# Kernel optimization log

Hardware: AMD Instinct MI355X
Metric: run time of the kernel (lower is better)

Reference implementation:

```python
import jax, jax.numpy as jnp
import numpy as np


def setup_inputs() -> dict:
    key = jax.random.key(0)
    ks = jax.random.split(key, 8)
    B, Cin, Cattr, Cout, H, W = 8, 256, 256, 256, 64, 64
    x = jax.random.normal(ks[0], (B, Cin, H, W), dtype=jnp.float32)
    attr = jax.random.normal(ks[1], (B, Cattr, H, W), dtype=jnp.float32)
    # 1x1 conv weights stored as [out, in] (kernel_size=1 squeezed)
    sq = 1.0 / np.sqrt(Cin)
    sa = 1.0 / np.sqrt(Cattr)
    Wq = jax.random.uniform(ks[2], (Cout, Cin), jnp.float32, -sq, sq)
    bq = jax.random.uniform(ks[3], (Cout,), jnp.float32, -sq, sq)
    Wk = jax.random.uniform(ks[4], (Cout, Cattr), jnp.float32, -sa, sa)
    bk = jax.random.uniform(ks[5], (Cout,), jnp.float32, -sa, sa)
    Wv = jax.random.uniform(ks[6], (Cout, Cattr), jnp.float32, -sa, sa)
    bv = jax.random.uniform(ks[7], (Cout,), jnp.float32, -sa, sa)
    return {"x": x, "attr": attr, "Wq": Wq, "bq": bq, "Wk": Wk, "bk": bk, "Wv": Wv, "bv": bv}


def reference(x, attr, Wq, bq, Wk, bk, Wv, bv):
    B, Cin, H, W = x.shape
    # 1x1 convs == per-pixel linear projections
    q = jnp.einsum('bchw,oc->bohw', x, Wq) + bq[None, :, None, None]      # [B,C,H,W]
    k = jnp.einsum('bchw,oc->bohw', attr, Wk) + bk[None, :, None, None]
    v = jnp.einsum('bchw,oc->bohw', attr, Wv) + bv[None, :, None, None]
    C = q.shape[1]
    qf = q.reshape(B, C, H * W)   # [B,C,N]
    kf = k.reshape(B, C, H * W)
    vf = v.reshape(B, C, H * W)
    # attn[b,i,j] = sum_c q[b,c,i] * k[b,c,j]  -> softmax over j
    attn = jax.nn.softmax(jnp.einsum('bci,bcj->bij', qf, kf), axis=-1)    # [B,N,N]
    out = jnp.einsum('bcj,bij->bci', vf, attn)                            # [B,C,N]
    return out.reshape(B, C, H, W) + x
```

## Files before the change

kernel.cpp:

```cpp
#include <hip/hip_runtime.h>

typedef _Float16 f16;
typedef _Float16 f16x8 __attribute__((ext_vector_type(8)));
typedef _Float16 f16x4 __attribute__((ext_vector_type(4)));
typedef float f32x4 __attribute__((ext_vector_type(4)));
typedef float f32x16 __attribute__((ext_vector_type(16)));

#define LOG2E 1.44269504088896340736f
#define SOFF  36.0f
#define CDIM 256
#define NPIX 4096

__device__ __forceinline__ void gl2lds16(const f16* g, const f16* l) {
    __builtin_amdgcn_global_load_lds((const __attribute__((address_space(1))) unsigned int*)g,
                                     (__attribute__((address_space(3))) unsigned int*)l, 16, 0, 0);
}

__global__ void convert_w_kernel(const float* __restrict__ Wq, const float* __restrict__ Wk,
                                 const float* __restrict__ Wv,
                                 f16* __restrict__ WqF, f16* __restrict__ WkF,
                                 f16* __restrict__ WvF) {
    int t = blockIdx.x * 256 + threadIdx.x;
    int m = t >> 13;
    int g = t & 8191;
    int lane = g & 63;
    int ksct = g >> 6;
    int ks = ksct & 15, ct = ksct >> 4;
    int o = ct * 32 + (lane & 31);
    int cin0 = ks * 16 + (lane >> 5) * 8;
    const float* W = (m == 0) ? Wq : ((m == 1) ? Wk : Wv);
    f16* WF = (m == 0) ? WqF : ((m == 1) ? WkF : WvF);
    const float scale = (m == 0) ? LOG2E : 1.0f;
    const float* src = W + (size_t)o * CDIM + cin0;
    f16x8 v;
#pragma unroll
    for (int e = 0; e < 8; ++e) v[e] = (f16)(src[e] * scale);
    *(f16x8*)(WF + (size_t)g * 8) = v;
}

__global__ __launch_bounds__(256, 2)
void proj_kernel(const float* __restrict__ x, const float* __restrict__ attr,
                 const f16* __restrict__ WqF, const float* __restrict__ bq,
                 const f16* __restrict__ WkF, const float* __restrict__ bk,
                 const f16* __restrict__ WvF, const float* __restrict__ bv,
                 f16* __restrict__ qT, f16* __restrict__ kT, f16* __restrict__ vF) {
    __shared__ __align__(16) f16 Xs[64 * 256];
    __shared__ __align__(16) f16 As[64 * 256];

    const int b  = blockIdx.x & 7;
    const int i0 = (blockIdx.x >> 3) * 64;
    const int t  = threadIdx.x;
    const int w = t >> 6, lane = t & 63, l31 = lane & 31, hi = lane >> 5;
    const int xorv = l31 & 7;

    {
        const int i  = t & 63;
        const int cb = t >> 6;
        const float* xb = x    + (size_t)b * CDIM * NPIX + i0 + i;
        const float* ab = attr + (size_t)b * CDIM * NPIX + i0 + i;
#pragma unroll 2
        for (int rep = 0; rep < 8; ++rep) {
            int chunk = cb * 8 + rep;
            const float* xs = xb + (size_t)(chunk * 8) * NPIX;
            const float* as_ = ab + (size_t)(chunk * 8) * NPIX;
            f16x8 xv, av;
#pragma unroll
            for (int e = 0; e < 8; ++e) {
                xv[e] = (f16)xs[(size_t)e * NPIX];
                av[e] = (f16)as_[(size_t)e * NPIX];
            }
            int phys = chunk ^ (i & 7);
            *(f16x8*)(Xs + i * 256 + phys * 8) = xv;
            *(f16x8*)(As + i * 256 + phys * 8) = av;
        }
    }
    __syncthreads();

#pragma unroll 1
    for (int k = 0; k < 12; ++k) {
        const int tt = w + 4 * k;
        const int kind = tt >> 4;
        const int rr = tt & 15;
        const int ct = rr >> 1;
        const int half = rr & 1;

        const f16* WF = (kind == 0) ? WqF : ((kind == 1) ? WkF : WvF);
        const f16* Bs = (kind == 0) ? Xs : As;
        const float* bias = (kind == 0) ? bq : ((kind == 1) ? bk : bv);
        const float bscale = (kind == 0) ? LOG2E : 1.0f;

        const f16* ap = WF + (size_t)(ct * 16) * 512 + (size_t)lane * 8;
        const f16* bp = Bs + (half * 32 + l31) * 256;

        f32x16 acc;
#pragma unroll
        for (int r = 0; r < 16; ++r) acc[r] = 0.0f;
#pragma unroll
        for (int ks = 0; ks < 16; ++ks) {
            f16x8 afr = *(const f16x8*)(ap + ks * 512);
            f16x8 bfr = *(const f16x8*)(bp + (((2 * ks + hi) ^ xorv)) * 8);
            acc = __builtin_amdgcn_mfma_f32_32x32x16_f16(afr, bfr, acc, 0, 0, 0);
        }

        const int nidx = i0 + half * 32 + l31;
        if (kind < 2) {
            f16* dst = ((kind == 0) ? qT : kT)
                       + ((size_t)b * NPIX + nidx) * CDIM + ct * 32 + 4 * hi;
#pragma unroll
            for (int g = 0; g < 4; ++g) {
                f32x4 bb = *(const f32x4*)(bias + ct * 32 + 4 * hi + 8 * g);
                f16x4 pk;
#pragma unroll
                for (int e = 0; e < 4; ++e) pk[e] = (f16)(acc[4 * g + e] + bb[e] * bscale);
                *(f16x4*)(dst + 8 * g) = pk;
            }
        } else {
            const int jpart = ((nidx >> 4) << 9) + (((nidx >> 3) & 1) << 8) + (nidx & 7);
            f16* vb2 = vF + (size_t)b * CDIM * NPIX + (size_t)ct * 131072 + jpart;
#pragma unroll
            for (int g = 0; g < 4; ++g) {
                f32x4 bb = *(const f32x4*)(bias + ct * 32 + 4 * hi + 8 * g);
#pragma unroll
                for (int e = 0; e < 4; ++e) {
                    int c31 = 4 * hi + 8 * g + e;
                    vb2[c31 * 8] = (f16)(acc[4 * g + e] + bb[e]);
                }
            }
        }
    }
}

__global__ __launch_bounds__(512, 2)
void attn_kernel(const f16* __restrict__ qT, const f16* __restrict__ kT,
                 const f16* __restrict__ vF, const float* __restrict__ x,
                 float* __restrict__ out) {
    extern __shared__ unsigned char smem[];

    const int b    = blockIdx.x & 7;
    const int i0   = (blockIdx.x >> 3) * 128;
    const int t    = threadIdx.x;
    const int w    = t >> 6;
    const int lane = t & 63;
    const int l31  = lane & 31;
    const int hi   = lane >> 5;
    const int iw   = (w & 3) * 32;
    const int jh   = (w >> 2) * 32;
    const int jh16 = (w >> 2) * 2;
    const int ig   = i0 + iw + l31;
    const int xorv = l31 & 7;

    f16x8 qf[16];
    {
        const f16* qp = qT + ((size_t)b * NPIX + ig) * CDIM + hi * 8;
#pragma unroll
        for (int ks = 0; ks < 16; ++ks) qf[ks] = *(const f16x8*)(qp + ks * 16);
    }

    int kp4o[4];
    {
        int kboff = (jh + l31) * 256 + (hi ^ (xorv & 1)) * 8;
        const int xv2 = xorv >> 1;
#pragma unroll
        for (int r = 0; r < 4; ++r) kp4o[r] = kboff + (r ^ xv2) * 16;
    }

    f32x16 acc[8];
#pragma unroll
    for (int ct = 0; ct < 8; ++ct)
#pragma unroll
        for (int r = 0; r < 16; ++r) acc[ct][r] = 0.0f;
    float lrun = 0.0f;

    const f16* kb  = kT + (size_t)b * NPIX * CDIM;
    const f16* vbJ = vF + (size_t)b * CDIM * NPIX;
    f16* lds0 = (f16*)smem;
    const int wub = (t & ~63) * 8;

    {
#pragma unroll
        for (int rep = 0; rep < 4; ++rep) {
            int slot = t + rep * 512;
            int krow = slot >> 5, kpc = slot & 31;
            gl2lds16(kb + (size_t)krow * CDIM + ((kpc ^ (krow & 7)) * 8),
                     lds0 + wub + rep * 4096);
        }
    }

    union Q4 { f16x4 h; unsigned int u[2]; };
    union B8 { f16x8 h; unsigned int u[4]; };

#pragma unroll 1
    for (int jt = 0; jt < 64; ++jt) {
        const int p = jt & 1;
        __syncthreads();

        const f16* vjt = vbJ + (size_t)jt * 2048 + (lane << 3) + (jh16 << 9);
        f16x8 vx0 = *(const f16x8*)(vjt);
        f16x8 vx1 = *(const f16x8*)(vjt + 512);
        f16x8 vy0 = *(const f16x8*)(vjt + 131072);
        f16x8 vy1 = *(const f16x8*)(vjt + 131072 + 512);

        if (jt < 63) {
            const int j0n = (jt + 1) * 64;
            f16* dstb = lds0 + (p ^ 1) * 16384;
#pragma unroll
            for (int rep = 0; rep < 4; ++rep) {
                int slot = t + rep * 512;
                int krow = slot >> 5, kpc = slot & 31;
                gl2lds16(kb + (size_t)(j0n + krow) * CDIM + ((kpc ^ (krow & 7)) * 8),
                         dstb + wub + rep * 4096);
            }
        }

        const f16* L = lds0 + p * 16384;

        f32x16 s;
#pragma unroll
        for (int r = 0; r < 16; ++r) s[r] = -SOFF;
#pragma unroll
        for (int ks = 0; ks < 16; ++ks)
            s = __builtin_amdgcn_mfma_f32_32x32x16_f16(
                *(const f16x8*)(L + kp4o[ks & 3] + (ks >> 2) * 64), qf[ks], s, 0, 0, 0);

        Q4 ownq[4];
        float rtot = 0.0f;
#pragma unroll
        for (int g = 0; g < 4; ++g) {
            float p0 = __builtin_amdgcn_exp2f(s[4 * g + 0]);
            float p1 = __builtin_amdgcn_exp2f(s[4 * g + 1]);
            float p2 = __builtin_amdgcn_exp2f(s[4 * g + 2]);
            float p3 = __builtin_amdgcn_exp2f(s[4 * g + 3]);
            rtot += (p0 + p1) + (p2 + p3);
            ownq[g].h[0] = (f16)p0; ownq[g].h[1] = (f16)p1;
            ownq[g].h[2] = (f16)p2; ownq[g].h[3] = (f16)p3;
        }
        lrun += rtot;

        f16x8 pb[2];
#pragma unroll
        for (int kj = 0; kj < 2; ++kj) {
            int sidx = 2 * kj + 1 - hi;
            int oidx = 2 * kj + hi;
            unsigned int s0 = ownq[sidx].u[0], s1 = ownq[sidx].u[1];
            unsigned int r0 = (unsigned int)__shfl_xor((int)s0, 32);
            unsigned int r1 = (unsigned int)__shfl_xor((int)s1, 32);
            B8 bb;
            bb.u[0] = hi ? r0 : ownq[oidx].u[0];
            bb.u[1] = hi ? r1 : ownq[oidx].u[1];
            bb.u[2] = hi ? ownq[oidx].u[0] : r0;
            bb.u[3] = hi ? ownq[oidx].u[1] : r1;
            pb[kj] = bb.h;
        }

#pragma unroll
        for (int ct = 0; ct < 8; ++ct) {
            f16x8 c0 = (ct & 1) ? vy0 : vx0;
            f16x8 c1 = (ct & 1) ? vy1 : vx1;
            if (ct < 6) {
                const f16* np = vjt + (size_t)(ct + 2) * 131072;
                f16x8 n0 = *(const f16x8*)(np);
                f16x8 n1 = *(const f16x8*)(np + 512);
                if (ct & 1) { vy0 = n0; vy1 = n1; } else { vx0 = n0; vx1 = n1; }
            }
            acc[ct] = __builtin_amdgcn_mfma_f32_32x32x16_f16(c0, pb[0], acc[ct], 0, 0, 0);
            acc[ct] = __builtin_amdgcn_mfma_f32_32x32x16_f16(c1, pb[1], acc[ct], 0, 0, 0);
        }
    }

    float lsum = lrun + __shfl_xor(lrun, 32);
    __syncthreads();
    float* Obuf = (float*)smem;
    float* Ls   = (float*)(smem + 131072);
    if (w >= 4) {
        float* ob = Obuf + (w - 4) * 8192;
#pragma unroll
        for (int ct = 0; ct < 8; ++ct)
#pragma unroll
            for (int r = 0; r < 16; ++r) {
                int c = ct * 32 + (r & 3) + 8 * (r >> 2) + 4 * hi;
                ob[c * 32 + l31] = acc[ct][r];
            }
        if (hi == 0) Ls[(w - 4) * 32 + l31] = lsum;
    }
    __syncthreads();
    if (w < 4) {
        const float ltot = lsum + Ls[w * 32 + l31];
        const float invl = 1.0f / ltot;
        const float* po = Obuf + w * 8192;
        const float* xb = x + (size_t)b * CDIM * NPIX + i0 + iw;
        float* og = out + (size_t)b * CDIM * NPIX + i0 + iw;
#pragma unroll
        for (int ct = 0; ct < 8; ++ct)
#pragma unroll
            for (int r = 0; r < 16; ++r) {
                int c = ct * 32 + (r & 3) + 8 * (r >> 2) + 4 * hi;
                size_t off = (size_t)c * NPIX + l31;
                og[off] = (acc[ct][r] + po[c * 32 + l31]) * invl + xb[off];
            }
    }
}

extern "C" void kernel_launch(void* const* d_in, const int* in_sizes, int n_in,
                              void* d_out, int out_size, void* d_ws, size_t ws_size,
                              hipStream_t stream) {
    const float* x    = (const float*)d_in[0];
    const float* attr = (const float*)d_in[1];
    const float* Wq   = (const float*)d_in[2];
    const float* bq   = (const float*)d_in[3];
    const float* Wk   = (const float*)d_in[4];
    const float* bk   = (const float*)d_in[5];
    const float* Wv   = (const float*)d_in[6];
    const float* bv   = (const float*)d_in[7];
    float* out = (float*)d_out;

    char* ws = (char*)d_ws;
    const size_t qkv_bytes = (size_t)8 * NPIX * CDIM * sizeof(f16);
    f16* qT   = (f16*)ws;
    f16* kT   = (f16*)(ws + qkv_bytes);
    f16* vF   = (f16*)(ws + 2 * qkv_bytes);
    f16* WqF  = (f16*)(ws + 3 * qkv_bytes);
    f16* WkF  = WqF + 65536;
    f16* WvF  = WkF + 65536;

    (void)hipFuncSetAttribute((const void*)attn_kernel,
                              hipFuncAttributeMaxDynamicSharedMemorySize, 131584);

    convert_w_kernel<<<96, 256, 0, stream>>>(Wq, Wk, Wv, WqF, WkF, WvF);
    proj_kernel<<<512, 256, 0, stream>>>(x, attr, WqF, bq, WkF, bk, WvF, bv, qT, kT, vF);
    attn_kernel<<<256, 512, 131584, stream>>>(qT, kT, vF, x, out);
}
```

Measured before the change: 326.8 us.

## Stage V tiles through LDS double buffer and widen swizzles

V is now stored row-major [C,N] and loaded into LDS with async global-to-LDS copies alongside K, double-buffered per tile, instead of each wave reading pre-fragmented V directly from global memory. The XOR swizzle widens to 32 columns for K and the projection operands to reduce LDS bank conflicts, and the projection epilogue stages results in LDS so global writes are coalesced 16-byte stores. s_setprio brackets the MFMA loops. This doubles the LDS footprint per stage (within the existing 131584-byte allocation) and adds LDS read traffic for V.

```diff
diff --git a/kernel.cpp b/kernel.cpp
--- a/kernel.cpp
+++ b/kernel.cpp
@@ -43,15 +43,17 @@
                  const f16* __restrict__ WqF, const float* __restrict__ bq,
                  const f16* __restrict__ WkF, const float* __restrict__ bk,
                  const f16* __restrict__ WvF, const float* __restrict__ bv,
-                 f16* __restrict__ qT, f16* __restrict__ kT, f16* __restrict__ vF) {
+                 f16* __restrict__ qT, f16* __restrict__ kT, f16* __restrict__ vW) {
     __shared__ __align__(16) f16 Xs[64 * 256];
     __shared__ __align__(16) f16 As[64 * 256];
+    __shared__ __align__(16) f16 Ostage[4][1024];
 
     const int b  = blockIdx.x & 7;
     const int i0 = (blockIdx.x >> 3) * 64;
     const int t  = threadIdx.x;
     const int w = t >> 6, lane = t & 63, l31 = lane & 31, hi = lane >> 5;
-    const int xorv = l31 & 7;
+    const int xu  = (l31 >> 1) & 15;
+    const int hib = (hi ^ (l31 & 1)) * 8;
 
     {
         const int i  = t & 63;
@@ -69,7 +71,7 @@
                 xv[e] = (f16)xs[(size_t)e * NPIX];
                 av[e] = (f16)as_[(size_t)e * NPIX];
             }
-            int phys = chunk ^ (i & 7);
+            int phys = chunk ^ (i & 31);
             *(f16x8*)(Xs + i * 256 + phys * 8) = xv;
             *(f16x8*)(As + i * 256 + phys * 8) = av;
         }
@@ -90,7 +92,7 @@
         const float bscale = (kind == 0) ? LOG2E : 1.0f;
 
         const f16* ap = WF + (size_t)(ct * 16) * 512 + (size_t)lane * 8;
-        const f16* bp = Bs + (half * 32 + l31) * 256;
+        const f16* bp = Bs + (half * 32 + l31) * 256 + hib;
 
         f32x16 acc;
 #pragma unroll
@@ -98,33 +100,47 @@
 #pragma unroll
         for (int ks = 0; ks < 16; ++ks) {
             f16x8 afr = *(const f16x8*)(ap + ks * 512);
-            f16x8 bfr = *(const f16x8*)(bp + (((2 * ks + hi) ^ xorv)) * 8);
+            f16x8 bfr = *(const f16x8*)(bp + ((ks ^ xu) << 4));
             acc = __builtin_amdgcn_mfma_f32_32x32x16_f16(afr, bfr, acc, 0, 0, 0);
         }
 
-        const int nidx = i0 + half * 32 + l31;
+        f16* st = Ostage[w];
         if (kind < 2) {
-            f16* dst = ((kind == 0) ? qT : kT)
-                       + ((size_t)b * NPIX + nidx) * CDIM + ct * 32 + 4 * hi;
 #pragma unroll
             for (int g = 0; g < 4; ++g) {
                 f32x4 bb = *(const f32x4*)(bias + ct * 32 + 4 * hi + 8 * g);
                 f16x4 pk;
 #pragma unroll
                 for (int e = 0; e < 4; ++e) pk[e] = (f16)(acc[4 * g + e] + bb[e] * bscale);
-                *(f16x4*)(dst + 8 * g) = pk;
+                *(f16x4*)(st + l31 * 32 + 4 * hi + 8 * g) = pk;
+            }
+            f16* dst = ((kind == 0) ? qT : kT)
+                       + ((size_t)b * NPIX + i0 + half * 32) * CDIM + ct * 32;
+#pragma unroll
+            for (int d = 0; d < 2; ++d) {
+                int row = d * 16 + (lane >> 2);
+                int c8  = (lane & 3) * 8;
+                f16x8 v = *(const f16x8*)(st + row * 32 + c8);
+                *(f16x8*)(dst + (size_t)row * CDIM + c8) = v;
             }
         } else {
-            const int jpart = ((nidx >> 4) << 9) + (((nidx >> 3) & 1) << 8) + (nidx & 7);
-            f16* vb2 = vF + (size_t)b * CDIM * NPIX + (size_t)ct * 131072 + jpart;
 #pragma unroll
             for (int g = 0; g < 4; ++g) {
                 f32x4 bb = *(const f32x4*)(bias + ct * 32 + 4 * hi + 8 * g);
 #pragma unroll
                 for (int e = 0; e < 4; ++e) {
                     int c31 = 4 * hi + 8 * g + e;
-                    vb2[c31 * 8] = (f16)(acc[4 * g + e] + bb[e]);
+                    st[c31 * 32 + l31] = (f16)(acc[4 * g + e] + bb[e]);
                 }
+            }
+            const int j0 = i0 + half * 32;
+            f16* dstb = vW + (size_t)b * CDIM * NPIX + (size_t)(ct * 32) * NPIX + j0;
+#pragma unroll
+            for (int d = 0; d < 2; ++d) {
+                int chunk = d * 64 + lane;
+                int c31 = chunk >> 2, jch = chunk & 3;
+                *(f16x8*)(dstb + (size_t)c31 * NPIX + jch * 8) =
+                    *(const f16x8*)(st + chunk * 8);
             }
         }
     }
@@ -132,7 +148,7 @@
 
 __global__ __launch_bounds__(512, 2)
 void attn_kernel(const f16* __restrict__ qT, const f16* __restrict__ kT,
-                 const f16* __restrict__ vF, const float* __restrict__ x,
+                 const f16* __restrict__ vW, const float* __restrict__ x,
                  float* __restrict__ out) {
     extern __shared__ unsigned char smem[];
 
@@ -145,9 +161,8 @@
     const int hi   = lane >> 5;
     const int iw   = (w & 3) * 32;
     const int jh   = (w >> 2) * 32;
-    const int jh16 = (w >> 2) * 2;
+    const int jh8  = (w >> 2) * 4;
     const int ig   = i0 + iw + l31;
-    const int xorv = l31 & 7;
 
     f16x8 qf[16];
     {
@@ -156,12 +171,14 @@
         for (int ks = 0; ks < 16; ++ks) qf[ks] = *(const f16x8*)(qp + ks * 16);
     }
 
-    int kp4o[4];
+    const int xu  = (l31 >> 1) & 15;
+    const int kbase = (jh + l31) * 256 + (hi ^ (l31 & 1)) * 8;
+    int vp2o[2];
     {
-        int kboff = (jh + l31) * 256 + (hi ^ (xorv & 1)) * 8;
-        const int xv2 = xorv >> 1;
-#pragma unroll
-        for (int r = 0; r < 4; ++r) kp4o[r] = kboff + (r ^ xv2) * 16;
+        int vbase = 16384 + (l31 >> 2) * 256 + (l31 & 3) * 64;
+#pragma unroll
+        for (int kj = 0; kj < 2; ++kj)
+            vp2o[kj] = vbase + (((jh8 + 2 * kj + hi) ^ (l31 & 7))) * 8;
     }
 
     f32x16 acc[8];
@@ -171,8 +188,8 @@
         for (int r = 0; r < 16; ++r) acc[ct][r] = 0.0f;
     float lrun = 0.0f;
 
-    const f16* kb  = kT + (size_t)b * NPIX * CDIM;
-    const f16* vbJ = vF + (size_t)b * CDIM * NPIX;
+    const f16* kb = kT + (size_t)b * NPIX * CDIM;
+    const f16* vb = vW + (size_t)b * CDIM * NPIX;
     f16* lds0 = (f16*)smem;
     const int wub = (t & ~63) * 8;
 
@@ -181,8 +198,13 @@
         for (int rep = 0; rep < 4; ++rep) {
             int slot = t + rep * 512;
             int krow = slot >> 5, kpc = slot & 31;
-            gl2lds16(kb + (size_t)krow * CDIM + ((kpc ^ (krow & 7)) * 8),
+            gl2lds16(kb + (size_t)krow * CDIM + ((kpc ^ (krow & 31)) * 8),
                      lds0 + wub + rep * 4096);
+            int R = slot >> 5, pv = slot & 31;
+            int vc = 4 * R + (pv >> 3);
+            int vjc = (pv & 7) ^ (vc & 7);
+            gl2lds16(vb + (size_t)vc * NPIX + vjc * 8,
+                     lds0 + 16384 + wub + rep * 4096);
         }
     }
 
@@ -194,33 +216,34 @@
         const int p = jt & 1;
         __syncthreads();
 
-        const f16* vjt = vbJ + (size_t)jt * 2048 + (lane << 3) + (jh16 << 9);
-        f16x8 vx0 = *(const f16x8*)(vjt);
-        f16x8 vx1 = *(const f16x8*)(vjt + 512);
-        f16x8 vy0 = *(const f16x8*)(vjt + 131072);
-        f16x8 vy1 = *(const f16x8*)(vjt + 131072 + 512);
-
         if (jt < 63) {
             const int j0n = (jt + 1) * 64;
-            f16* dstb = lds0 + (p ^ 1) * 16384;
+            f16* dstb = lds0 + (p ^ 1) * 32768;
 #pragma unroll
             for (int rep = 0; rep < 4; ++rep) {
                 int slot = t + rep * 512;
                 int krow = slot >> 5, kpc = slot & 31;
-                gl2lds16(kb + (size_t)(j0n + krow) * CDIM + ((kpc ^ (krow & 7)) * 8),
+                gl2lds16(kb + (size_t)(j0n + krow) * CDIM + ((kpc ^ (krow & 31)) * 8),
                          dstb + wub + rep * 4096);
-            }
-        }
-
-        const f16* L = lds0 + p * 16384;
+                int R = slot >> 5, pv = slot & 31;
+                int vc = 4 * R + (pv >> 3);
+                int vjc = (pv & 7) ^ (vc & 7);
+                gl2lds16(vb + (size_t)vc * NPIX + j0n + vjc * 8,
+                         dstb + 16384 + wub + rep * 4096);
+            }
+        }
+
+        const f16* L = lds0 + p * 32768;
 
         f32x16 s;
 #pragma unroll
         for (int r = 0; r < 16; ++r) s[r] = -SOFF;
+        __builtin_amdgcn_s_setprio(1);
 #pragma unroll
         for (int ks = 0; ks < 16; ++ks)
             s = __builtin_amdgcn_mfma_f32_32x32x16_f16(
-                *(const f16x8*)(L + kp4o[ks & 3] + (ks >> 2) * 64), qf[ks], s, 0, 0, 0);
+                *(const f16x8*)(L + kbase + ((ks ^ xu) << 4)), qf[ks], s, 0, 0, 0);
+        __builtin_amdgcn_s_setprio(0);
 
         Q4 ownq[4];
         float rtot = 0.0f;
@@ -252,19 +275,15 @@
             pb[kj] = bb.h;
         }
 
+        __builtin_amdgcn_s_setprio(1);
 #pragma unroll
         for (int ct = 0; ct < 8; ++ct) {
-            f16x8 c0 = (ct & 1) ? vy0 : vx0;
-            f16x8 c1 = (ct & 1) ? vy1 : vx1;
-            if (ct < 6) {
-                const f16* np = vjt + (size_t)(ct + 2) * 131072;
-                f16x8 n0 = *(const f16x8*)(np);
-                f16x8 n1 = *(const f16x8*)(np + 512);
-                if (ct & 1) { vy0 = n0; vy1 = n1; } else { vx0 = n0; vx1 = n1; }
-            }
-            acc[ct] = __builtin_amdgcn_mfma_f32_32x32x16_f16(c0, pb[0], acc[ct], 0, 0, 0);
-            acc[ct] = __builtin_amdgcn_mfma_f32_32x32x16_f16(c1, pb[1], acc[ct], 0, 0, 0);
-        }
+            acc[ct] = __builtin_amdgcn_mfma_f32_32x32x16_f16(
+                *(const f16x8*)(L + vp2o[0] + ct * 2048), pb[0], acc[ct], 0, 0, 0);
+            acc[ct] = __builtin_amdgcn_mfma_f32_32x32x16_f16(
+                *(const f16x8*)(L + vp2o[1] + ct * 2048), pb[1], acc[ct], 0, 0, 0);
+        }
+        __builtin_amdgcn_s_setprio(0);
     }
 
     float lsum = lrun + __shfl_xor(lrun, 32);
@@ -317,7 +336,7 @@
     const size_t qkv_bytes = (size_t)8 * NPIX * CDIM * sizeof(f16);
     f16* qT   = (f16*)ws;
     f16* kT   = (f16*)(ws + qkv_bytes);
-    f16* vF   = (f16*)(ws + 2 * qkv_bytes);
+    f16* vW   = (f16*)(ws + 2 * qkv_bytes);
     f16* WqF  = (f16*)(ws + 3 * qkv_bytes);
     f16* WkF  = WqF + 65536;
     f16* WvF  = WkF + 65536;
@@ -326,6 +345,6 @@
                               hipFuncAttributeMaxDynamicSharedMemorySize, 131584);
 
     convert_w_kernel<<<96, 256, 0, stream>>>(Wq, Wk, Wv, WqF, WkF, WvF);
-    proj_kernel<<<512, 256, 0, stream>>>(x, attr, WqF, bq, WkF, bk, WvF, bv, qT, kT, vF);
-    attn_kernel<<<256, 512, 131584, stream>>>(qT, kT, vF, x, out);
-}
+    proj_kernel<<<512, 256, 0, stream>>>(x, attr, WqF, bq, WkF, bk, WvF, bv, qT, kT, vW);
+    attn_kernel<<<256, 512, 131584, stream>>>(qT, kT, vW, x, out);
+}
```

New measurement: 332.4 us. Within noise of the previous version (+1.7%).
